# Optimization experiments

Hardware: AMD Instinct MI355X
Metric: run time of the kernel (lower is better)

Reference implementation:

```python
import jax, jax.numpy as jnp
import numpy as np

B, N, C, NF = 4, 512, 128, 96
NUM_OPS = 1

def setup_inputs() -> dict:
    key = jax.random.key(0)
    ks = jax.random.split(key, 11)
    x = jax.random.normal(ks[0], (B, N, C), dtype=jnp.float32)
    # W_id is the per-batch identity mask [B, N, N, 1]
    W_id = jnp.broadcast_to(jnp.eye(N, dtype=jnp.float32)[None, :, :, None], (B, N, N, 1))
    def lin(k, out_c, in_c):
        return jax.random.normal(k, (out_c, in_c), dtype=jnp.float32) / np.sqrt(in_c).astype(np.float32)
    w1 = lin(ks[1], 2 * NF, C);  b1 = jnp.zeros((2 * NF,), jnp.float32)
    w2 = lin(ks[2], 2 * NF, 2 * NF); b2 = jnp.zeros((2 * NF,), jnp.float32)
    w3 = lin(ks[3], NF, 2 * NF); b3 = jnp.zeros((NF,), jnp.float32)
    w4 = lin(ks[4], NF, NF);     b4 = jnp.zeros((NF,), jnp.float32)
    w5 = lin(ks[5], NUM_OPS, NF); b5 = jnp.zeros((NUM_OPS,), jnp.float32)
    return {"x": x, "W_id": W_id, "w1": w1, "b1": b1, "w2": w2, "b2": b2,
            "w3": w3, "b3": b3, "w4": w4, "b4": b4, "w5": w5, "b5": b5}

def _conv1x1(h, w, b):
    # 1x1 conv over channel-last edge tensor [B, N, N, Cin] -> [B, N, N, Cout]
    return jnp.einsum('bijc,oc->bijo', h, w) + b

def reference(x, W_id, w1, b1, w2, b2, w3, b3, w4, b4, w5, b5):
    lrelu = lambda t: jax.nn.leaky_relu(t, negative_slope=0.01)
    # pairwise abs-diff edge features [B, N, N, C]
    d = jnp.abs(x[:, :, None, :] - x[:, None, :, :])
    h = lrelu(_conv1x1(d, w1, b1))
    h = lrelu(_conv1x1(h, w2, b2))
    h = lrelu(_conv1x1(h, w3, b3))
    h = lrelu(_conv1x1(h, w4, b4))
    W = _conv1x1(h, w5, b5)          # [B, N, N, 1]
    W = W - W_id * 1e8               # mask self-edges with large negative
    W = jax.nn.softmax(W, axis=2)    # softmax over neighbor axis (dim 2)
    return jnp.concatenate([W_id, W], axis=3)  # operator 'J2' -> [B, N, N, 2]
```

## Files before the change

kernel.cpp:

```cpp
#include <hip/hip_runtime.h>
#include <hip/hip_bf16.h>

#define NB 4
#define NN 512
#define CC 128

typedef __bf16 bf16x8 __attribute__((ext_vector_type(8)));
typedef __bf16 bf16x4 __attribute__((ext_vector_type(4)));
typedef float  f32x4  __attribute__((ext_vector_type(4)));
typedef int    i32x8  __attribute__((ext_vector_type(8)));

#define SCL 0x7F7F7F7F

__device__ __forceinline__ void barrier_lds() {
    __builtin_amdgcn_s_waitcnt(0xC07F);
    __builtin_amdgcn_fence(__ATOMIC_RELEASE, "workgroup", "local");
    __builtin_amdgcn_s_barrier();
    __builtin_amdgcn_fence(__ATOMIC_ACQUIRE, "workgroup", "local");
}

__device__ __forceinline__ float lrelu(float v) { return fmaxf(v, 0.01f * v); }

__device__ __forceinline__ int pk4(float a, float b, float c, float d) {
    int p = __builtin_amdgcn_cvt_pk_fp8_f32(a, b, 0, false);
    return  __builtin_amdgcn_cvt_pk_fp8_f32(c, d, p, true);
}

__device__ __forceinline__ i32x8 ld_lds32(const unsigned char* p) {
    i32x8 r;
    long long* q = (long long*)&r;
    q[0] = *(const long long*)(p);
    q[1] = *(const long long*)(p + 8);
    q[2] = *(const long long*)(p + 16);
    q[3] = *(const long long*)(p + 24);
    return r;
}

__global__ void cvt_all(const float* __restrict__ x,  __bf16* __restrict__ xb,
                        const float* __restrict__ w1, int* __restrict__ w1f,
                        const float* __restrict__ w2, int* __restrict__ w2f,
                        const float* __restrict__ w3, int* __restrict__ w3f,
                        const float* __restrict__ w4, unsigned char* __restrict__ w4fp)
{
    int idx = blockIdx.x * blockDim.x + threadIdx.x;
    if (idx < 65536) {
        float4 v = ((const float4*)x)[idx];
        bf16x4 o = { (__bf16)v.x, (__bf16)v.y, (__bf16)v.z, (__bf16)v.w };
        ((bf16x4*)xb)[idx] = o;
    } else if (idx < 85504) {
        const float* s; int* d; int off;
        if      (idx < 71680) { s = w1; d = w1f; off = idx - 65536; }
        else if (idx < 80896) { s = w2; d = w2f; off = idx - 71680; }
        else                  { s = w3; d = w3f; off = idx - 80896; }
        float4 v = ((const float4*)s)[off];
        d[off] = pk4(v.x, v.y, v.z, v.w);
    } else if (idx < 87808) {
        int off = idx - 85504;
        int r = off / 24, c = (off % 24) * 4;
        float4 v = ((const float4*)w4)[off];
        *(int*)(w4fp + r * 128 + c) = pk4(v.x, v.y, v.z, v.w);
    } else if (idx < 88000) {
        int p = idx - 87808;
        int r = p >> 1;
        *(int4*)(w4fp + r * 128 + 96 + (p & 1) * 16) = make_int4(0, 0, 0, 0);
    }
}

__global__ __launch_bounds__(256, 3) void mlp_edges(
    const __bf16* __restrict__ xb,
    const unsigned char* __restrict__ w1p, const float* __restrict__ b1,
    const unsigned char* __restrict__ w2p, const float* __restrict__ b2,
    const unsigned char* __restrict__ w3p, const float* __restrict__ b3,
    const unsigned char* __restrict__ w4p, const float* __restrict__ b4,
    const float* __restrict__ w5,  const float* __restrict__ b5,
    float* __restrict__ out)
{
    __shared__ __align__(16) unsigned char AbufB[128 * 200];
    __shared__ __align__(16) unsigned char BbufB[128 * 200];
    __shared__ float red[256];

    const int t = threadIdx.x;
    const int lane = t & 63, wave = t >> 6;
    const int l15 = lane & 15, q = lane >> 4, q8 = q * 8, q32 = q * 32;
    const int j0 = blockIdx.x * 16, i0 = blockIdx.y * 8, b = blockIdx.z;

    i32x8 w1v[3]; f32x4 b1v[3];
#pragma unroll
    for (int u = 0; u < 3; ++u) {
        const int ch = (wave + u * 4) * 16;
        b1v[u] = *(const f32x4*)(b1 + ch + q * 4);
        w1v[u] = *(const i32x8*)(w1p + (size_t)(ch + l15) * 128 + q32);
    }
    __builtin_amdgcn_sched_barrier(0);

    {
        const int m = t >> 1, c0 = (t & 1) * 64;
        const __bf16* xi = xb + ((size_t)b * NN + (i0 + (m >> 4))) * CC + c0;
        const __bf16* xj = xb + ((size_t)b * NN + (j0 + (m & 15))) * CC + c0;
        unsigned char* drow = AbufB + m * 136 + c0;
#pragma unroll
        for (int h = 0; h < 4; ++h) {
            bf16x8 a0  = *(const bf16x8*)(xi + h * 16);
            bf16x8 a1  = *(const bf16x8*)(xi + h * 16 + 8);
            bf16x8 c0v = *(const bf16x8*)(xj + h * 16);
            bf16x8 c1v = *(const bf16x8*)(xj + h * 16 + 8);
            float dv[16];
#pragma unroll
            for (int u = 0; u < 8; ++u) {
                dv[u]     = fabsf((float)a0[u] - (float)c0v[u]);
                dv[u + 8] = fabsf((float)a1[u] - (float)c1v[u]);
            }
            int2 lo = make_int2(pk4(dv[0], dv[1], dv[2],  dv[3]),
                                pk4(dv[4], dv[5], dv[6],  dv[7]));
            int2 hi = make_int2(pk4(dv[8], dv[9], dv[10], dv[11]),
                                pk4(dv[12], dv[13], dv[14], dv[15]));
            *(int2*)(drow + h * 16)     = lo;
            *(int2*)(drow + h * 16 + 8) = hi;
        }
    }

    barrier_lds();

#pragma unroll
    for (int nt = 0; nt < 8; ++nt) {
        i32x8 bfs = ld_lds32(AbufB + (nt * 16 + l15) * 136 + q32);
        f32x4 acc[3] = { b1v[0], b1v[1], b1v[2] };
#pragma unroll
        for (int u = 0; u < 3; ++u)
            acc[u] = __builtin_amdgcn_mfma_scale_f32_16x16x128_f8f6f4(
                         w1v[u], bfs, acc[u], 0, 0, 0, SCL, 0, SCL);
        unsigned char* orow = BbufB + (nt * 16 + l15) * 200 + q * 4;
#pragma unroll
        for (int u = 0; u < 3; ++u)
            *(int*)(orow + (wave + u * 4) * 16) =
                pk4(lrelu(acc[u][0]), lrelu(acc[u][1]), lrelu(acc[u][2]), lrelu(acc[u][3]));
    }

    i32x8 w2s[3]; long long w2r[3][2]; f32x4 b2v[3];
#pragma unroll
    for (int u = 0; u < 3; ++u) {
        const int ch = (wave + u * 4) * 16;
        b2v[u] = *(const f32x4*)(b2 + ch + q * 4);
        const unsigned char* wrow = w2p + (size_t)(ch + l15) * 192;
        w2s[u] = *(const i32x8*)(wrow + q32);
        w2r[u][0] = *(const long long*)(wrow + 128 + q8);
        w2r[u][1] = *(const long long*)(wrow + 160 + q8);
    }
    __builtin_amdgcn_sched_barrier(0);

    barrier_lds();

#pragma unroll
    for (int nt = 0; nt < 8; ++nt) {
        const unsigned char* inrow = BbufB + (nt * 16 + l15) * 200;
        i32x8 bfs = ld_lds32(inrow + q32);
        long long bfr0 = *(const long long*)(inrow + 128 + q8);
        long long bfr1 = *(const long long*)(inrow + 160 + q8);
        f32x4 acc[3] = { b2v[0], b2v[1], b2v[2] };
#pragma unroll
        for (int u = 0; u < 3; ++u) {
            acc[u] = __builtin_amdgcn_mfma_scale_f32_16x16x128_f8f6f4(
                         w2s[u], bfs, acc[u], 0, 0, 0, SCL, 0, SCL);
            acc[u] = __builtin_amdgcn_mfma_f32_16x16x32_fp8_fp8(w2r[u][0], bfr0, acc[u], 0, 0, 0);
            acc[u] = __builtin_amdgcn_mfma_f32_16x16x32_fp8_fp8(w2r[u][1], bfr1, acc[u], 0, 0, 0);
        }
        unsigned char* orow = AbufB + (nt * 16 + l15) * 200 + q * 4;
#pragma unroll
        for (int u = 0; u < 3; ++u)
            *(int*)(orow + (wave + u * 4) * 16) =
                pk4(lrelu(acc[u][0]), lrelu(acc[u][1]), lrelu(acc[u][2]), lrelu(acc[u][3]));
    }

    const int mc0n = (wave & 1) * 3;
    const int nlo  = (wave >> 1) * 4;
    i32x8 w3s[3]; long long w3r[3][2]; f32x4 b3v[3];
#pragma unroll
    for (int u = 0; u < 3; ++u) {
        const int ch = (mc0n + u) * 16;
        b3v[u] = *(const f32x4*)(b3 + ch + q * 4);
        const unsigned char* wrow = w3p + (size_t)(ch + l15) * 192;
        w3s[u] = *(const i32x8*)(wrow + q32);
        w3r[u][0] = *(const long long*)(wrow + 128 + q8);
        w3r[u][1] = *(const long long*)(wrow + 160 + q8);
    }
    __builtin_amdgcn_sched_barrier(0);

    barrier_lds();

    {
        unsigned char* pz = BbufB + (t >> 1) * 136 + 96 + (t & 1) * 16;
        *(long long*)(pz)     = 0;
        *(long long*)(pz + 8) = 0;
    }

#pragma unroll
    for (int ntl = 0; ntl < 4; ++ntl) {
        const int nt = nlo + ntl;
        const unsigned char* inrow = AbufB + (nt * 16 + l15) * 200;
        i32x8 bfs = ld_lds32(inrow + q32);
        long long bfr0 = *(const long long*)(inrow + 128 + q8);
        long long bfr1 = *(const long long*)(inrow + 160 + q8);
        f32x4 acc[3] = { b3v[0], b3v[1], b3v[2] };
#pragma unroll
        for (int u = 0; u < 3; ++u) {
            acc[u] = __builtin_amdgcn_mfma_scale_f32_16x16x128_f8f6f4(
                         w3s[u], bfs, acc[u], 0, 0, 0, SCL, 0, SCL);
            acc[u] = __builtin_amdgcn_mfma_f32_16x16x32_fp8_fp8(w3r[u][0], bfr0, acc[u], 0, 0, 0);
            acc[u] = __builtin_amdgcn_mfma_f32_16x16x32_fp8_fp8(w3r[u][1], bfr1, acc[u], 0, 0, 0);
        }
        unsigned char* orow = BbufB + (nt * 16 + l15) * 136 + q * 4;
#pragma unroll
        for (int u = 0; u < 3; ++u)
            *(int*)(orow + (mc0n + u) * 16) =
                pk4(lrelu(acc[u][0]), lrelu(acc[u][1]), lrelu(acc[u][2]), lrelu(acc[u][3]));
    }

    i32x8 w4s[3]; f32x4 b4v[3], w5v[3];
#pragma unroll
    for (int u = 0; u < 3; ++u) {
        const int ch = (mc0n + u) * 16;
        b4v[u] = *(const f32x4*)(b4 + ch + q * 4);
        w5v[u] = *(const f32x4*)(w5 + ch + q * 4);
        w4s[u] = *(const i32x8*)(w4p + (size_t)(ch + l15) * 128 + q32);
    }
    __builtin_amdgcn_sched_barrier(0);

    barrier_lds();

#pragma unroll
    for (int ntl = 0; ntl < 4; ++ntl) {
        const int nt = nlo + ntl;
        i32x8 bfs = ld_lds32(BbufB + (nt * 16 + l15) * 136 + q32);
        f32x4 acc[3] = { b4v[0], b4v[1], b4v[2] };
#pragma unroll
        for (int u = 0; u < 3; ++u)
            acc[u] = __builtin_amdgcn_mfma_scale_f32_16x16x128_f8f6f4(
                         w4s[u], bfs, acc[u], 0, 0, 0, SCL, 0, SCL);
        float p = 0.f;
#pragma unroll
        for (int u = 0; u < 3; ++u)
#pragma unroll
            for (int r = 0; r < 4; ++r)
                p += lrelu(acc[u][r]) * w5v[u][r];
        p += __shfl_xor(p, 16, 64);
        p += __shfl_xor(p, 32, 64);
        if (q == 0) red[(wave * 4 + ntl) * 16 + l15] = p;
    }

    barrier_lds();

    if (t < 128) {
        const int tile = t >> 4, e = t & 15;
        const int pair = tile >> 2, tl = tile & 3;
        const float logit = red[((pair * 2 + 0) * 4 + tl) * 16 + e]
                          + red[((pair * 2 + 1) * 4 + tl) * 16 + e] + b5[0];
        const int i = i0 + tile;
        const int j = j0 + e;
        out[(((size_t)b * NN + i) * NN + j) * 2 + 1] = logit;
    }
}

__global__ __launch_bounds__(256) void softmax_rows(float* __restrict__ out)
{
    const int row = blockIdx.x;
    const int i   = row & (NN - 1);
    float* base = out + (size_t)row * (NN * 2);
    const int t = threadIdx.x;

    float v0 = base[t * 2 + 1];
    float v1 = base[(t + 256) * 2 + 1];
    if (t == i)       v0 = -__builtin_inff();
    if (t + 256 == i) v1 = -__builtin_inff();

    float mx = fmaxf(v0, v1);
#pragma unroll
    for (int off = 32; off; off >>= 1) mx = fmaxf(mx, __shfl_xor(mx, off, 64));
    __shared__ float sm[4], ss[4];
    const int wave = t >> 6, lane = t & 63;
    if (lane == 0) sm[wave] = mx;
    __syncthreads();
    mx = fmaxf(fmaxf(sm[0], sm[1]), fmaxf(sm[2], sm[3]));

    const float e0 = __expf(v0 - mx), e1 = __expf(v1 - mx);
    float s = e0 + e1;
#pragma unroll
    for (int off = 32; off; off >>= 1) s += __shfl_xor(s, off, 64);
    if (lane == 0) ss[wave] = s;
    __syncthreads();
    s = ss[0] + ss[1] + ss[2] + ss[3];
    const float inv = 1.0f / s;

    float2* o2 = (float2*)base;
    o2[t]       = make_float2(t == i ? 1.f : 0.f,         e0 * inv);
    o2[t + 256] = make_float2((t + 256) == i ? 1.f : 0.f, e1 * inv);
}

extern "C" void kernel_launch(void* const* d_in, const int* in_sizes, int n_in,
                              void* d_out, int out_size, void* d_ws, size_t ws_size,
                              hipStream_t stream) {
    const float* x  = (const float*)d_in[0];
    const float* w1 = (const float*)d_in[2];
    const float* b1 = (const float*)d_in[3];
    const float* w2 = (const float*)d_in[4];
    const float* b2 = (const float*)d_in[5];
    const float* w3 = (const float*)d_in[6];
    const float* b3 = (const float*)d_in[7];
    const float* w4 = (const float*)d_in[8];
    const float* b4 = (const float*)d_in[9];
    const float* w5 = (const float*)d_in[10];
    const float* b5 = (const float*)d_in[11];
    float* out = (float*)d_out;

    char* ws = (char*)d_ws;
    __bf16*        xb   = (__bf16*)(ws);
    unsigned char* w1f  = (unsigned char*)(ws + 524288);
    unsigned char* w2f  = (unsigned char*)(ws + 548864);
    unsigned char* w3f  = (unsigned char*)(ws + 585728);
    unsigned char* w4fp = (unsigned char*)(ws + 604160);

    cvt_all<<<(88000 + 255) / 256, 256, 0, stream>>>(x, xb, w1, (int*)w1f,
                                                     w2, (int*)w2f, w3, (int*)w3f,
                                                     w4, w4fp);

    dim3 grid(NN / 16, NN / 8, NB);
    mlp_edges<<<grid, 256, 0, stream>>>(xb, w1f, b1, w2f, b2, w3f, b3, w4fp, b4,
                                        w5, b5, out);

    softmax_rows<<<NB * NN, 256, 0, stream>>>(out);
}
```

Baseline: 249.1 us.

## Pad LDS rows to 16-byte strides, widen LDS accesses, pack leaky-relu math

New measurement: 252.5 us. Within noise of the previous version (+1.3%).

```diff
diff --git a/kernel.cpp b/kernel.cpp
--- a/kernel.cpp
+++ b/kernel.cpp
@@ -7,7 +7,9 @@
 
 typedef __bf16 bf16x8 __attribute__((ext_vector_type(8)));
 typedef __bf16 bf16x4 __attribute__((ext_vector_type(4)));
+typedef float  f32x2  __attribute__((ext_vector_type(2)));
 typedef float  f32x4  __attribute__((ext_vector_type(4)));
+typedef int    i32x4  __attribute__((ext_vector_type(4)));
 typedef int    i32x8  __attribute__((ext_vector_type(8)));
 
 #define SCL 0x7F7F7F7F
@@ -19,20 +21,24 @@
     __builtin_amdgcn_fence(__ATOMIC_ACQUIRE, "workgroup", "local");
 }
 
-__device__ __forceinline__ float lrelu(float v) { return fmaxf(v, 0.01f * v); }
-
 __device__ __forceinline__ int pk4(float a, float b, float c, float d) {
     int p = __builtin_amdgcn_cvt_pk_fp8_f32(a, b, 0, false);
     return  __builtin_amdgcn_cvt_pk_fp8_f32(c, d, p, true);
 }
 
+__device__ __forceinline__ int pk_lrelu(f32x4 a) {
+    f32x2 lo = {a[0], a[1]}, hi = {a[2], a[3]};
+    f32x2 llo = __builtin_elementwise_max(lo, lo * 0.01f);
+    f32x2 lhi = __builtin_elementwise_max(hi, hi * 0.01f);
+    int p = __builtin_amdgcn_cvt_pk_fp8_f32(llo[0], llo[1], 0, false);
+    return  __builtin_amdgcn_cvt_pk_fp8_f32(lhi[0], lhi[1], p, true);
+}
+
 __device__ __forceinline__ i32x8 ld_lds32(const unsigned char* p) {
     i32x8 r;
-    long long* q = (long long*)&r;
-    q[0] = *(const long long*)(p);
-    q[1] = *(const long long*)(p + 8);
-    q[2] = *(const long long*)(p + 16);
-    q[3] = *(const long long*)(p + 24);
+    i32x4* q = (i32x4*)&r;
+    q[0] = *(const i32x4*)(p);
+    q[1] = *(const i32x4*)(p + 16);
     return r;
 }
 
@@ -75,9 +81,9 @@
     const float* __restrict__ w5,  const float* __restrict__ b5,
     float* __restrict__ out)
 {
-    __shared__ __align__(16) unsigned char AbufB[128 * 200];
-    __shared__ __align__(16) unsigned char BbufB[128 * 200];
-    __shared__ float red[256];
+    __shared__ __align__(16) unsigned char AbufB[128 * 208];
+    __shared__ __align__(16) unsigned char BbufB[128 * 208];
+    float* const red = (float*)AbufB;
 
     const int t = threadIdx.x;
     const int lane = t & 63, wave = t >> 6;
@@ -97,7 +103,7 @@
         const int m = t >> 1, c0 = (t & 1) * 64;
         const __bf16* xi = xb + ((size_t)b * NN + (i0 + (m >> 4))) * CC + c0;
         const __bf16* xj = xb + ((size_t)b * NN + (j0 + (m & 15))) * CC + c0;
-        unsigned char* drow = AbufB + m * 136 + c0;
+        unsigned char* drow = AbufB + m * 144 + c0;
 #pragma unroll
         for (int h = 0; h < 4; ++h) {
             bf16x8 a0  = *(const bf16x8*)(xi + h * 16);
@@ -110,12 +116,12 @@
                 dv[u]     = fabsf((float)a0[u] - (float)c0v[u]);
                 dv[u + 8] = fabsf((float)a1[u] - (float)c1v[u]);
             }
-            int2 lo = make_int2(pk4(dv[0], dv[1], dv[2],  dv[3]),
-                                pk4(dv[4], dv[5], dv[6],  dv[7]));
-            int2 hi = make_int2(pk4(dv[8], dv[9], dv[10], dv[11]),
-                                pk4(dv[12], dv[13], dv[14], dv[15]));
-            *(int2*)(drow + h * 16)     = lo;
-            *(int2*)(drow + h * 16 + 8) = hi;
+            int4 pk;
+            pk.x = pk4(dv[0], dv[1], dv[2],  dv[3]);
+            pk.y = pk4(dv[4], dv[5], dv[6],  dv[7]);
+            pk.z = pk4(dv[8], dv[9], dv[10], dv[11]);
+            pk.w = pk4(dv[12], dv[13], dv[14], dv[15]);
+            *(int4*)(drow + h * 16) = pk;
         }
     }
 
@@ -123,17 +129,14 @@
 
 #pragma unroll
     for (int nt = 0; nt < 8; ++nt) {
-        i32x8 bfs = ld_lds32(AbufB + (nt * 16 + l15) * 136 + q32);
-        f32x4 acc[3] = { b1v[0], b1v[1], b1v[2] };
-#pragma unroll
-        for (int u = 0; u < 3; ++u)
-            acc[u] = __builtin_amdgcn_mfma_scale_f32_16x16x128_f8f6f4(
-                         w1v[u], bfs, acc[u], 0, 0, 0, SCL, 0, SCL);
-        unsigned char* orow = BbufB + (nt * 16 + l15) * 200 + q * 4;
-#pragma unroll
-        for (int u = 0; u < 3; ++u)
-            *(int*)(orow + (wave + u * 4) * 16) =
-                pk4(lrelu(acc[u][0]), lrelu(acc[u][1]), lrelu(acc[u][2]), lrelu(acc[u][3]));
+        i32x8 bfs = ld_lds32(AbufB + (nt * 16 + l15) * 144 + q32);
+        unsigned char* orow = BbufB + (nt * 16 + l15) * 208 + q * 4;
+#pragma unroll
+        for (int u = 0; u < 3; ++u) {
+            f32x4 acc = __builtin_amdgcn_mfma_scale_f32_16x16x128_f8f6f4(
+                            w1v[u], bfs, b1v[u], 0, 0, 0, SCL, 0, SCL);
+            *(int*)(orow + (wave + u * 4) * 16) = pk_lrelu(acc);
+        }
     }
 
     i32x8 w2s[3]; long long w2r[3][2]; f32x4 b2v[3];
@@ -152,23 +155,19 @@
 
 #pragma unroll
     for (int nt = 0; nt < 8; ++nt) {
-        const unsigned char* inrow = BbufB + (nt * 16 + l15) * 200;
+        const unsigned char* inrow = BbufB + (nt * 16 + l15) * 208;
         i32x8 bfs = ld_lds32(inrow + q32);
         long long bfr0 = *(const long long*)(inrow + 128 + q8);
         long long bfr1 = *(const long long*)(inrow + 160 + q8);
-        f32x4 acc[3] = { b2v[0], b2v[1], b2v[2] };
+        unsigned char* orow = AbufB + (nt * 16 + l15) * 208 + q * 4;
 #pragma unroll
         for (int u = 0; u < 3; ++u) {
-            acc[u] = __builtin_amdgcn_mfma_scale_f32_16x16x128_f8f6f4(
-                         w2s[u], bfs, acc[u], 0, 0, 0, SCL, 0, SCL);
-            acc[u] = __builtin_amdgcn_mfma_f32_16x16x32_fp8_fp8(w2r[u][0], bfr0, acc[u], 0, 0, 0);
-            acc[u] = __builtin_amdgcn_mfma_f32_16x16x32_fp8_fp8(w2r[u][1], bfr1, acc[u], 0, 0, 0);
-        }
-        unsigned char* orow = AbufB + (nt * 16 + l15) * 200 + q * 4;
-#pragma unroll
-        for (int u = 0; u < 3; ++u)
-            *(int*)(orow + (wave + u * 4) * 16) =
-                pk4(lrelu(acc[u][0]), lrelu(acc[u][1]), lrelu(acc[u][2]), lrelu(acc[u][3]));
+            f32x4 acc = __builtin_amdgcn_mfma_scale_f32_16x16x128_f8f6f4(
+                            w2s[u], bfs, b2v[u], 0, 0, 0, SCL, 0, SCL);
+            acc = __builtin_amdgcn_mfma_f32_16x16x32_fp8_fp8(w2r[u][0], bfr0, acc, 0, 0, 0);
+            acc = __builtin_amdgcn_mfma_f32_16x16x32_fp8_fp8(w2r[u][1], bfr1, acc, 0, 0, 0);
+            *(int*)(orow + (wave + u * 4) * 16) = pk_lrelu(acc);
+        }
     }
 
     const int mc0n = (wave & 1) * 3;
@@ -187,32 +186,24 @@
 
     barrier_lds();
 
-    {
-        unsigned char* pz = BbufB + (t >> 1) * 136 + 96 + (t & 1) * 16;
-        *(long long*)(pz)     = 0;
-        *(long long*)(pz + 8) = 0;
-    }
+    *(int4*)(BbufB + (t >> 1) * 144 + 96 + (t & 1) * 16) = make_int4(0, 0, 0, 0);
 
 #pragma unroll
     for (int ntl = 0; ntl < 4; ++ntl) {
         const int nt = nlo + ntl;
-        const unsigned char* inrow = AbufB + (nt * 16 + l15) * 200;
+        const unsigned char* inrow = AbufB + (nt * 16 + l15) * 208;
         i32x8 bfs = ld_lds32(inrow + q32);
         long long bfr0 = *(const long long*)(inrow + 128 + q8);
         long long bfr1 = *(const long long*)(inrow + 160 + q8);
-        f32x4 acc[3] = { b3v[0], b3v[1], b3v[2] };
+        unsigned char* orow = BbufB + (nt * 16 + l15) * 144 + q * 4;
 #pragma unroll
         for (int u = 0; u < 3; ++u) {
-            acc[u] = __builtin_amdgcn_mfma_scale_f32_16x16x128_f8f6f4(
-                         w3s[u], bfs, acc[u], 0, 0, 0, SCL, 0, SCL);
-            acc[u] = __builtin_amdgcn_mfma_f32_16x16x32_fp8_fp8(w3r[u][0], bfr0, acc[u], 0, 0, 0);
-            acc[u] = __builtin_amdgcn_mfma_f32_16x16x32_fp8_fp8(w3r[u][1], bfr1, acc[u], 0, 0, 0);
-        }
-        unsigned char* orow = BbufB + (nt * 16 + l15) * 136 + q * 4;
-#pragma unroll
-        for (int u = 0; u < 3; ++u)
-            *(int*)(orow + (mc0n + u) * 16) =
-                pk4(lrelu(acc[u][0]), lrelu(acc[u][1]), lrelu(acc[u][2]), lrelu(acc[u][3]));
+            f32x4 acc = __builtin_amdgcn_mfma_scale_f32_16x16x128_f8f6f4(
+                            w3s[u], bfs, b3v[u], 0, 0, 0, SCL, 0, SCL);
+            acc = __builtin_amdgcn_mfma_f32_16x16x32_fp8_fp8(w3r[u][0], bfr0, acc, 0, 0, 0);
+            acc = __builtin_amdgcn_mfma_f32_16x16x32_fp8_fp8(w3r[u][1], bfr1, acc, 0, 0, 0);
+            *(int*)(orow + (mc0n + u) * 16) = pk_lrelu(acc);
+        }
     }
 
     i32x8 w4s[3]; f32x4 b4v[3], w5v[3];
@@ -230,18 +221,19 @@
 #pragma unroll
     for (int ntl = 0; ntl < 4; ++ntl) {
         const int nt = nlo + ntl;
-        i32x8 bfs = ld_lds32(BbufB + (nt * 16 + l15) * 136 + q32);
-        f32x4 acc[3] = { b4v[0], b4v[1], b4v[2] };
-#pragma unroll
-        for (int u = 0; u < 3; ++u)
-            acc[u] = __builtin_amdgcn_mfma_scale_f32_16x16x128_f8f6f4(
-                         w4s[u], bfs, acc[u], 0, 0, 0, SCL, 0, SCL);
-        float p = 0.f;
-#pragma unroll
-        for (int u = 0; u < 3; ++u)
-#pragma unroll
-            for (int r = 0; r < 4; ++r)
-                p += lrelu(acc[u][r]) * w5v[u][r];
+        i32x8 bfs = ld_lds32(BbufB + (nt * 16 + l15) * 144 + q32);
+        f32x2 p2 = {0.f, 0.f};
+#pragma unroll
+        for (int u = 0; u < 3; ++u) {
+            f32x4 acc = __builtin_amdgcn_mfma_scale_f32_16x16x128_f8f6f4(
+                            w4s[u], bfs, b4v[u], 0, 0, 0, SCL, 0, SCL);
+            f32x2 lo = {acc[0], acc[1]}, hi = {acc[2], acc[3]};
+            lo = __builtin_elementwise_max(lo, lo * 0.01f);
+            hi = __builtin_elementwise_max(hi, hi * 0.01f);
+            f32x2 w5lo = {w5v[u][0], w5v[u][1]}, w5hi = {w5v[u][2], w5v[u][3]};
+            p2 += lo * w5lo + hi * w5hi;
+        }
+        float p = p2[0] + p2[1];
         p += __shfl_xor(p, 16, 64);
         p += __shfl_xor(p, 32, 64);
         if (q == 0) red[(wave * 4 + ntl) * 16 + l15] = p;
```
